# Performance work log

Measured on AMD Instinct MI355X. Metric: run time of the kernel, lower is better.

Reference implementation:

```python
import jax, jax.numpy as jnp
import numpy as np

C = 128; HEADS = 8; GH = 32; GW = 32; B = 8; PD = 8  # PD = (dim//4)//4

def _conv(x, w, pad, dil=1, groups=1):
    return jax.lax.conv_general_dilated(
        x, w, (1, 1), [(pad[0], pad[0]), (pad[1], pad[1])],
        rhs_dilation=(dil, dil),
        dimension_numbers=('NCHW', 'OIHW', 'NCHW'),
        feature_group_count=groups)

def _lrelu(t):
    return jnp.where(t >= 0, t, 0.1 * t)

def _ln(t, g, b, eps=1e-5):
    m = jnp.mean(t, -1, keepdims=True)
    v = jnp.var(t, -1, keepdims=True)
    return (t - m) * jax.lax.rsqrt(v + eps) * g + b

def setup_inputs():
    rng = np.random.RandomState(0)
    f = lambda *s: jnp.asarray((rng.randn(*s) * 0.05).astype(np.float32))
    ones = lambda n: jnp.ones((n,), jnp.float32)
    zeros = lambda n: jnp.zeros((n,), jnp.float32)
    # Swin-style relative position index over the (GH, GW) group
    coords = np.stack(np.meshgrid(np.arange(GH), np.arange(GW), indexing='ij')).reshape(2, -1)
    rel = (coords[:, :, None] - coords[:, None, :]).transpose(1, 2, 0)
    rel[..., 0] += GH - 1; rel[..., 1] += GW - 1; rel[..., 0] *= 2 * GW - 1
    rel_idx = jnp.asarray(rel.sum(-1).astype(np.int32))  # [N, N]
    biases = np.stack(np.meshgrid(np.arange(1 - GH, GH), np.arange(1 - GW, GW), indexing='ij'))
    biases = jnp.asarray(biases.reshape(2, -1).T.astype(np.float32))  # [(2GH-1)*(2GW-1), 2]
    return dict(
        x=jnp.asarray(rng.rand(B, C, GH, GW).astype(np.float32)),
        conv1_w=f(C, C, 3, 3), conv2_w=f(C, C, 3, 3), conv3_w=f(C, C, 3, 3),
        convt_w=f(C, 3, 1, 1),
        rba_w=f(C, C, 3, 1), rba_b=zeros(C), rbb_w=f(C, C, 1, 3), rbb_b=zeros(C),
        pp_w=f(PD, 2), pp_b=zeros(PD),
        l1_g=ones(PD), l1_b=zeros(PD), l1_w=f(PD, PD), l1_b2=zeros(PD),
        l2_g=ones(PD), l2_b=zeros(PD), l2_w=f(PD, PD), l2_b2=zeros(PD),
        l3_g=ones(PD), l3_b=zeros(PD), l3_w=f(HEADS, PD), l3_b2=zeros(HEADS),
        qk_w=f(2 * C, C), qk_b=zeros(2 * C),
        v_w=f(C, C), v_b=zeros(C),
        proj_w=f(C, C), proj_b=zeros(C),
        fc1_w=f(C, C), fc1_b=zeros(C), fc2_w=f(C, C), fc2_b=zeros(C),
        biases=biases, rel_idx=rel_idx,
    )

def reference(x, conv1_w, conv2_w, conv3_w, convt_w, rba_w, rba_b, rbb_w, rbb_b,
              pp_w, pp_b, l1_g, l1_b, l1_w, l1_b2, l2_g, l2_b, l2_w, l2_b2,
              l3_g, l3_b, l3_w, l3_b2, qk_w, qk_b, v_w, v_b, proj_w, proj_b,
              fc1_w, fc1_b, fc2_w, fc2_b, biases, rel_idx):
    Bn, Cc, Hh, Ww = x.shape
    N = Hh * Ww
    hd = Cc // HEADS
    # FeaExtract: ResASPP (3 dilated 3x3 convs, grouped 1x1 merge) + residual
    b1 = _lrelu(_conv(x, conv1_w, (1, 1)))
    b2 = _lrelu(_conv(x, conv2_w, (3, 3), dil=3))
    b3 = _lrelu(_conv(x, conv3_w, (5, 5), dil=5))
    a = _conv(jnp.concatenate([b1, b2, b3], 1), convt_w, (0, 0), groups=Cc) + x
    # RB: (3,1) conv -> lrelu -> (1,3) conv + residual
    r = _lrelu(_conv(a, rba_w, (1, 0)) + rba_b[None, :, None, None])
    r = _conv(r, rbb_w, (0, 1)) + rbb_b[None, :, None, None]
    o0 = r + a
    # original uses in-place clamp_, so o0 is clamped before flattening
    o0 = jnp.clip(o0, 0.0, 1.0)
    E = o0.reshape(Bn, Cc, N).transpose(0, 2, 1)  # [B, N, C]
    qk = E @ qk_w.T + qk_b  # [B, N, 2C]
    q = qk[..., :Cc].reshape(Bn, N, HEADS, hd).transpose(0, 2, 1, 3)
    k = qk[..., Cc:].reshape(Bn, N, HEADS, hd).transpose(0, 2, 1, 3)
    v = (E @ v_w.T + v_b).reshape(Bn, N, HEADS, hd).transpose(0, 2, 1, 3)
    attn = jnp.einsum('bhid,bhjd->bhij', q * (hd ** -0.5), k)
    # DynamicPosBias MLP (residual=False): Linear(2,pd) -> [LN,ReLU,Linear] x2 -> LN,ReLU,Linear(pd,heads)
    p = biases @ pp_w.T + pp_b
    p = jax.nn.relu(_ln(p, l1_g, l1_b)) @ l1_w.T + l1_b2
    p = jax.nn.relu(_ln(p, l2_g, l2_b)) @ l2_w.T + l2_b2
    p = jax.nn.relu(_ln(p, l3_g, l3_b)) @ l3_w.T + l3_b2  # [L, heads]
    rpb = p[rel_idx]  # gather -> [N, N, heads]
    attn = attn + rpb.transpose(2, 0, 1)[None]
    attn = jax.nn.softmax(attn, axis=-1)
    y = jnp.einsum('bhij,bhjd->bhid', attn, v).transpose(0, 2, 1, 3).reshape(Bn, N, Cc) + E
    x_proj = y @ proj_w.T + proj_b
    h = jax.nn.gelu(x_proj @ fc1_w.T + fc1_b, approximate=False)
    return (h @ fc2_w.T + fc2_b) + y
```

## Files before the change

kernel.cpp:

```cpp
#include <hip/hip_runtime.h>
#include <hip/hip_bf16.h>

typedef __hip_bfloat16 bf16;
typedef __bf16 bf16x8 __attribute__((ext_vector_type(8)));
typedef float f32x4 __attribute__((ext_vector_type(4)));
typedef __fp16 f16x2 __attribute__((ext_vector_type(2)));
typedef __fp16 f16x4 __attribute__((ext_vector_type(4)));

#define Lb 3969

#define XP_F   0
#define WF_F   903168
#define WR_F   1124352
#define WG_F   1173504
#define BH_F   1222656
#define R1P_F  1222656
#define QKV_F  1222656
#define AP_F   2795520
#define YT_F   2795520
#define EB_F   3352576
#define XPT_F  3352576
#define H1T_F  0
#define RPB_F  3876864
#define FLAG_F 3908616
#define RT_F   3908624
#define VT_F   4924432

__device__ __forceinline__ float b2f(bf16 v) { return __bfloat162float(v); }
__device__ __forceinline__ bf16 f2b(float v) { return __float2bfloat16(v); }

template <typename T> __device__ __forceinline__ float ldw(const void* p, int i);
template <> __device__ __forceinline__ float ldw<bf16>(const void* p, int i) {
  return __bfloat162float(((const bf16*)p)[i]);
}
template <> __device__ __forceinline__ float ldw<float>(const void* p, int i) {
  return ((const float*)p)[i];
}
template <typename T> __device__ __forceinline__ void stw(void* p, size_t i, float v);
template <> __device__ __forceinline__ void stw<bf16>(void* p, size_t i, float v) {
  ((bf16*)p)[i] = __float2bfloat16(v);
}
template <> __device__ __forceinline__ void stw<float>(void* p, size_t i, float v) {
  ((float*)p)[i] = v;
}

__device__ __forceinline__ unsigned pkb(float a, float b) {
  bf16 x = __float2bfloat16(a), y = __float2bfloat16(b);
  unsigned short ux = *(unsigned short*)&x, uy = *(unsigned short*)&y;
  return (unsigned)ux | ((unsigned)uy << 16);
}
__device__ __forceinline__ unsigned pkh(float a, float b) {
  f16x2 t = __builtin_amdgcn_cvt_pkrtz(a, b);
  return *(unsigned*)&t;
}

__device__ __forceinline__ bool detect_local(const unsigned* x) {
  int lane = threadIdx.x & 63;
  int cnt = 0;
#pragma unroll
  for (int k = 0; k < 4; ++k) {
    unsigned lo = x[lane + 64 * k] & 0xFFFFu;
    cnt += (lo >= 0x3C00u && lo < 0x3F80u) ? 1 : 0;
  }
#pragma unroll
  for (int off = 1; off < 64; off <<= 1) cnt += __shfl_xor(cnt, off);
  return cnt >= 128;
}

template <typename T>
__device__ void wprep_all_body(const void* w1, const void* w2, const void* w3,
                               const void* rba_w, const void* rbb_w,
                               const void* qk_w, const void* v_w,
                               const void* proj_w, const void* fc1_w,
                               const void* fc2_w, bf16* __restrict__ Wf,
                               bf16* __restrict__ Wr, bf16* __restrict__ Wg)
{
  int tid = blockIdx.x * 256 + threadIdx.x;
  int lane = tid & 63, li = lane & 15, quad = lane >> 4;
  if (tid < 55296) {
    int mt = (tid >> 6) & 7;
    int Kc = (tid >> 9) & 3;
    int rem = tid >> 11;
    int t = rem % 9;
    int br = rem / 9;
    const void* w = (br == 0 ? w1 : (br == 1 ? w2 : w3));
    int o = mt * 16 + li;
    int ci0 = Kc * 32 + quad * 8;
#pragma unroll
    for (int j = 0; j < 8; ++j)
      Wf[(size_t)tid * 8 + j] = f2b(ldw<T>(w, (o * 128 + ci0 + j) * 9 + t));
  } else {
    int u = tid - 55296;
    if (u < 12288) {
      int Kc = (u >> 6) & 3, mt = (u >> 8) & 7, q = u >> 11;
      const void* w = (q >= 3) ? rbb_w : rba_w;
      int t = q % 3;
#pragma unroll
      for (int j = 0; j < 8; ++j)
        Wr[(size_t)u * 8 + j] =
            f2b(ldw<T>(w, ((mt * 16 + li) * 128 + Kc * 32 + quad * 8 + j) * 3 + t));
    } else if (u < 24576) {
      int g = u - 12288;
      int Kc = (g >> 6) & 3, mtg = g >> 8;
      const void* w; int mrow; float sc = 1.f;
      if (mtg < 16)      { w = qk_w;   mrow = mtg * 16; if (mtg < 8) sc = 0.25f; }
      else if (mtg < 24) { w = v_w;    mrow = (mtg - 16) * 16; }
      else if (mtg < 32) { w = proj_w; mrow = (mtg - 24) * 16; }
      else if (mtg < 40) { w = fc1_w;  mrow = (mtg - 32) * 16; }
      else               { w = fc2_w;  mrow = (mtg - 40) * 16; }
#pragma unroll
      for (int j = 0; j < 8; ++j)
        Wg[(size_t)g * 8 + j] =
            f2b(sc * ldw<T>(w, (mrow + li) * 128 + Kc * 32 + quad * 8 + j));
    }
  }
}

__global__ __launch_bounds__(256) void wprep_all_kernel(
    const unsigned* x, const void* w1, const void* w2, const void* w3,
    const void* rba_w, const void* rbb_w, const void* qk_w, const void* v_w,
    const void* proj_w, const void* fc1_w, const void* fc2_w,
    bf16* Wf, bf16* Wr, bf16* Wg, int* flag)
{
  bool isbf = detect_local(x);
  if (blockIdx.x == 0 && threadIdx.x == 0) *flag = isbf ? 1 : 0;
  if (isbf) wprep_all_body<bf16>(w1, w2, w3, rba_w, rbb_w, qk_w, v_w, proj_w,
                                 fc1_w, fc2_w, Wf, Wr, Wg);
  else      wprep_all_body<float>(w1, w2, w3, rba_w, rbb_w, qk_w, v_w, proj_w,
                                  fc1_w, fc2_w, Wf, Wr, Wg);
}

template <typename T>
__device__ void nhwc_body(const void* x, bf16* __restrict__ xp, bf16 (*tile)[128])
{
  const int b = blockIdx.x >> 5;
  const int row = blockIdx.x & 31;
  const int t = threadIdx.x;
  const size_t bbase = (size_t)b * 42 * 42 * 128;
  const bf16x8 z = (bf16x8){};

  if (t < 160) {
    int side = t / 80;
    int off = (t % 80) * 8;
    *(bf16x8*)&xp[bbase + ((size_t)(row + 5) * 42 + side * 37) * 128 + off] = z;
  }
  {
    int zr = (row < 5) ? row : ((row >= 27) ? row + 10 : -1);
    if (zr >= 0) {
      size_t base = bbase + (size_t)zr * 42 * 128;
      for (int k = t; k < 672; k += 256) *(bf16x8*)&xp[base + k * 8] = z;
    }
  }

  {
    int ci = t >> 1, half = t & 1;
#pragma unroll
    for (int j = 0; j < 16; ++j) {
      int px = half * 16 + j;
      tile[px][ci] = f2b(ldw<T>(x, ((size_t)b * 128 + ci) * 1024 + row * 32 + px));
    }
  }
  __syncthreads();
  {
    int px = t >> 3, c0 = (t & 7) * 16;
    bf16* dst = xp + (bbase + ((size_t)(row + 5) * 42 + (px + 5)) * 128 + c0);
#pragma unroll
    for (int j = 0; j < 16; ++j) dst[j] = tile[px][c0 + j];
  }
}

__global__ __launch_bounds__(256) void nhwc_kernel(const void* x, bf16* xp,
                                                   const int* flag)
{
  __shared__ bf16 tile[32][128];
  if (*flag) nhwc_body<bf16>(x, xp, tile);
  else       nhwc_body<float>(x, xp, tile);
}

__global__ __launch_bounds__(256) void aspp2_kernel(
    const bf16* __restrict__ xp, const bf16* __restrict__ Wf,
    bf16* __restrict__ bh)
{
  const int nt_ = blockIdx.x, br = blockIdx.y >> 1, mh = blockIdx.y & 1;
  const int bb = blockIdx.z;
  const int w = threadIdx.x >> 6, lane = threadIdx.x & 63;
  const int quad = lane >> 4, li = lane & 15;
  const int d = (br == 0 ? 1 : (br == 1 ? 3 : 5));
  const int pxw = nt_ * 64 + w * 16;
  const int y = pxw >> 5, xb = pxw & 31;

  f32x4 acc[4] = {};
  const bf16* Wbase = Wf + (size_t)br * 18432 * 8 + (size_t)mh * 4 * 64 * 8;

  for (int t = 0; t < 9; ++t) {
    const int dy = (t / 3 - 1) * d, dx = (t % 3 - 1) * d;
    const bf16* Asite =
        xp + (((size_t)bb * 42 + (y + 5 + dy)) * 42 + (xb + li + 5 + dx)) * 128;
    const bf16* Wt = Wbase + (size_t)t * 2048 * 8;
#pragma unroll
    for (int Kc = 0; Kc < 4; ++Kc) {
      bf16x8 afrag = *(const bf16x8*)(Asite + Kc * 32 + quad * 8);
      const bf16* Wk = Wt + (size_t)Kc * 512 * 8 + (size_t)lane * 8;
#pragma unroll
      for (int mt = 0; mt < 4; ++mt) {
        bf16x8 wfrag = *(const bf16x8*)(Wk + (size_t)mt * 64 * 8);
        acc[mt] = __builtin_amdgcn_mfma_f32_16x16x32_bf16(afrag, wfrag, acc[mt],
                                                          0, 0, 0);
      }
    }
  }
#pragma unroll
  for (int mt = 0; mt < 4; ++mt)
#pragma unroll
    for (int r = 0; r < 4; ++r) {
      int px = pxw + quad * 4 + r;
      bh[((size_t)bb * 1024 + px) * 384 + br * 128 + (mh * 4 + mt) * 16 + li] =
          f2b(acc[mt][r]);
    }
}

template <typename T>
__device__ void merge2_body(const bf16* __restrict__ xp, const void* wt,
                            const bf16* __restrict__ bh, bf16* __restrict__ ap,
                            float* cw)
{
  const int b = blockIdx.y, px0 = blockIdx.x * 32;
  const bf16x8 z = (bf16x8){};
  if (blockIdx.x == 0) {
    size_t base = ((size_t)b * 34 + 0) * 32 * 128;
    for (int k = threadIdx.x; k < 512; k += 256) *(bf16x8*)&ap[base + k * 8] = z;
  } else if (blockIdx.x == 31) {
    size_t base = ((size_t)b * 34 + 33) * 32 * 128;
    for (int k = threadIdx.x; k < 512; k += 256) *(bf16x8*)&ap[base + k * 8] = z;
  }
  for (int i = threadIdx.x; i < 384; i += 256) cw[i] = ldw<T>(wt, i);
  __syncthreads();
  const int pxl = threadIdx.x >> 3, og = threadIdx.x & 7;
  const int px = px0 + pxl, o0 = og * 16;
  const int y = px >> 5, x = px & 31;
  const bf16* brow = bh + ((size_t)b * 1024 + px) * 384 + o0 * 3;
  const bf16* xrow = xp + (((size_t)b * 42 + y + 5) * 42 + x + 5) * 128 + o0;
  bf16* arow = ap + (((size_t)b * 34 + y + 1) * 32 + x) * 128 + o0;

  bf16 bl[48], xl[16], ol[16];
#pragma unroll
  for (int k = 0; k < 6; ++k) *(bf16x8*)&bl[k * 8] = *(const bf16x8*)&brow[k * 8];
  *(bf16x8*)&xl[0] = *(const bf16x8*)&xrow[0];
  *(bf16x8*)&xl[8] = *(const bf16x8*)&xrow[8];
#pragma unroll
  for (int j = 0; j < 16; ++j) {
    float v = b2f(xl[j]);
#pragma unroll
    for (int i = 0; i < 3; ++i) {
      float t = b2f(bl[j * 3 + i]);
      v += cw[(o0 + j) * 3 + i] * (t >= 0.f ? t : 0.1f * t);
    }
    ol[j] = f2b(v);
  }
  *(bf16x8*)&arow[0] = *(bf16x8*)&ol[0];
  *(bf16x8*)&arow[8] = *(bf16x8*)&ol[8];
}

__global__ __launch_bounds__(256) void merge2_kernel(
    const bf16* xp, const void* wt, const bf16* bh, bf16* ap, const int* flag)
{
  __shared__ float cw[384];
  if (*flag) merge2_body<bf16>(xp, wt, bh, ap, cw);
  else       merge2_body<float>(xp, wt, bh, ap, cw);
}

template <typename T>
__device__ void rb1_body(const bf16* __restrict__ ap, const bf16* __restrict__ Wr,
                         const void* bias, bf16* __restrict__ r1p)
{
  const int b = blockIdx.z, mh = blockIdx.y;
  const int lane = threadIdx.x;
  const int quad = lane >> 4, li = lane & 15;
  const int pxw = blockIdx.x * 16;
  const int y = pxw >> 5, xb = pxw & 31;
  f32x4 acc[4] = {};
#pragma unroll
  for (int t = 0; t < 3; ++t) {
    const bf16* Asite = ap + (((size_t)b * 34 + y + t) * 32 + xb + li) * 128;
#pragma unroll
    for (int Kc = 0; Kc < 4; ++Kc) {
      bf16x8 afrag = *(const bf16x8*)(Asite + Kc * 32 + quad * 8);
#pragma unroll
      for (int mt = 0; mt < 4; ++mt) {
        int f = (t * 8 + mh * 4 + mt) * 4 + Kc;
        bf16x8 wfrag = *(const bf16x8*)(Wr + ((size_t)f * 64 + lane) * 8);
        acc[mt] = __builtin_amdgcn_mfma_f32_16x16x32_bf16(afrag, wfrag, acc[mt],
                                                          0, 0, 0);
      }
    }
  }
  if (quad == 0) {
    int xcol = (xb == 0) ? 0 : 33;
#pragma unroll
    for (int mt = 0; mt < 4; ++mt)
      r1p[(((size_t)b * 32 + y) * 34 + xcol) * 128 + (mh * 4 + mt) * 16 + li] =
          f2b(0.f);
  }
#pragma unroll
  for (int mt = 0; mt < 4; ++mt) {
    int o = (mh * 4 + mt) * 16 + li;
    float bv = ldw<T>(bias, o);
#pragma unroll
    for (int r = 0; r < 4; ++r) {
      int x = xb + quad * 4 + r;
      float v = acc[mt][r] + bv;
      v = (v >= 0.f ? v : 0.1f * v);
      r1p[(((size_t)b * 32 + y) * 34 + x + 1) * 128 + o] = f2b(v);
    }
  }
}

__global__ __launch_bounds__(64) void rb1_kernel(
    const bf16* ap, const bf16* Wr, const void* bias, bf16* r1p, const int* flag)
{
  if (*flag) rb1_body<bf16>(ap, Wr, bias, r1p);
  else       rb1_body<float>(ap, Wr, bias, r1p);
}

template <typename T>
__device__ void rb2_body(const bf16* __restrict__ r1p, const bf16* __restrict__ Wr,
                         const void* bias, const bf16* __restrict__ ap,
                         bf16* __restrict__ Eb)
{
  const int b = blockIdx.z, mh = blockIdx.y;
  const int lane = threadIdx.x;
  const int quad = lane >> 4, li = lane & 15;
  const int pxw = blockIdx.x * 16;
  const int y = pxw >> 5, xb = pxw & 31;
  f32x4 acc[4] = {};
#pragma unroll
  for (int t = 0; t < 3; ++t) {
    const bf16* Asite = r1p + (((size_t)b * 32 + y) * 34 + xb + li + t) * 128;
#pragma unroll
    for (int Kc = 0; Kc < 4; ++Kc) {
      bf16x8 afrag = *(const bf16x8*)(Asite + Kc * 32 + quad * 8);
#pragma unroll
      for (int mt = 0; mt < 4; ++mt) {
        int f = ((3 + t) * 8 + mh * 4 + mt) * 4 + Kc;
        bf16x8 wfrag = *(const bf16x8*)(Wr + ((size_t)f * 64 + lane) * 8);
        acc[mt] = __builtin_amdgcn_mfma_f32_16x16x32_bf16(afrag, wfrag, acc[mt],
                                                          0, 0, 0);
      }
    }
  }
#pragma unroll
  for (int mt = 0; mt < 4; ++mt) {
    int o = (mh * 4 + mt) * 16 + li;
    float bv = ldw<T>(bias, o);
#pragma unroll
    for (int r = 0; r < 4; ++r) {
      int x = xb + quad * 4 + r;
      float v = acc[mt][r] + bv +
                b2f(ap[(((size_t)b * 34 + y + 1) * 32 + x) * 128 + o]);
      v = fminf(fmaxf(v, 0.f), 1.f);
      Eb[((size_t)b * 1024 + y * 32 + x) * 128 + o] = f2b(v);
    }
  }
}

__global__ __launch_bounds__(64) void rb2_kernel(
    const bf16* r1p, const bf16* Wr, const void* bias, const bf16* ap,
    bf16* Eb, const int* flag)
{
  if (*flag) rb2_body<bf16>(r1p, Wr, bias, ap, Eb);
  else       rb2_body<float>(r1p, Wr, bias, ap, Eb);
}

template <typename T>
__device__ __forceinline__ void ln_relu8(const float* t, float* u,
                                         const void* g, const void* bb)
{
  float m = 0.f;
#pragma unroll
  for (int k = 0; k < 8; ++k) m += t[k];
  m *= 0.125f;
  float v = 0.f;
#pragma unroll
  for (int k = 0; k < 8; ++k) { float d = t[k] - m; v += d * d; }
  v *= 0.125f;
  float r = rsqrtf(v + 1e-5f);
#pragma unroll
  for (int k = 0; k < 8; ++k) {
    float val = (t[k] - m) * r * ldw<T>(g, k) + ldw<T>(bb, k);
    u[k] = val > 0.f ? val : 0.f;
  }
}

template <typename T>
__device__ void dpb_body(const void* biases, const void* pp_w, const void* pp_b,
                         const void* l1_g, const void* l1_b, const void* l1_w,
                         const void* l1_b2, const void* l2_g, const void* l2_b,
                         const void* l2_w, const void* l2_b2, const void* l3_g,
                         const void* l3_b, const void* l3_w, const void* l3_b2,
                         float* __restrict__ RPB)
{
  int r = blockIdx.x * 256 + threadIdx.x;
  if (r >= Lb) return;
  float b0 = ldw<T>(biases, r * 2), b1 = ldw<T>(biases, r * 2 + 1);
  float t[8], u[8];
#pragma unroll
  for (int j = 0; j < 8; ++j)
    t[j] = b0 * ldw<T>(pp_w, j * 2) + b1 * ldw<T>(pp_w, j * 2 + 1) +
           ldw<T>(pp_b, j);
  ln_relu8<T>(t, u, l1_g, l1_b);
#pragma unroll
  for (int j = 0; j < 8; ++j) {
    float s = ldw<T>(l1_b2, j);
#pragma unroll
    for (int k = 0; k < 8; ++k) s += u[k] * ldw<T>(l1_w, j * 8 + k);
    t[j] = s;
  }
  ln_relu8<T>(t, u, l2_g, l2_b);
#pragma unroll
  for (int j = 0; j < 8; ++j) {
    float s = ldw<T>(l2_b2, j);
#pragma unroll
    for (int k = 0; k < 8; ++k) s += u[k] * ldw<T>(l2_w, j * 8 + k);
    t[j] = s;
  }
  ln_relu8<T>(t, u, l3_g, l3_b);
#pragma unroll
  for (int h = 0; h < 8; ++h) {
    float s = ldw<T>(l3_b2, h);
#pragma unroll
    for (int k = 0; k < 8; ++k) s += u[k] * ldw<T>(l3_w, h * 8 + k);
    RPB[h * Lb + r] = s;
  }
}

__global__ __launch_bounds__(256) void dpb_kernel(
    const void* biases, const void* pp_w, const void* pp_b, const void* l1_g,
    const void* l1_b, const void* l1_w, const void* l1_b2, const void* l2_g,
    const void* l2_b, const void* l2_w, const void* l2_b2, const void* l3_g,
    const void* l3_b, const void* l3_w, const void* l3_b2, float* RPB,
    const int* flag)
{
  if (*flag)
    dpb_body<bf16>(biases, pp_w, pp_b, l1_g, l1_b, l1_w, l1_b2, l2_g, l2_b,
                   l2_w, l2_b2, l3_g, l3_b, l3_w, l3_b2, RPB);
  else
    dpb_body<float>(biases, pp_w, pp_b, l1_g, l1_b, l1_w, l1_b2, l2_g, l2_b,
                    l2_w, l2_b2, l3_g, l3_b, l3_w, l3_b2, RPB);
}

__global__ __launch_bounds__(64) void rt_kernel(
    const float* __restrict__ RPB, float* __restrict__ RTf)
{
  const int tt = blockIdx.x, h = blockIdx.y;
  const int t = tt >> 1, p = tt & 1;
  const int lane = threadIdx.x, quad = lane >> 4, li = lane & 15;
  const float* rp = RPB + h * Lb;
  float* dst = RTf + ((size_t)(h * 124 + tt) * 4) * 256 + lane * 4;
#pragma unroll
  for (int mt = 0; mt < 4; ++mt) {
    f32x4 v;
#pragma unroll
    for (int r = 0; r < 4; ++r) {
      int j = mt * 16 + quad * 4 + r;
      int dy = (t - 30) - (j >> 5);
      int dx = (p * 16 + li) - (j & 31);
      v[r] = rp[(dy + 31) * 63 + dx + 31];
    }
    *(f32x4*)(dst + mt * 256) = v;
  }
}

__global__ __launch_bounds__(64) void vt_kernel(
    const bf16* __restrict__ QKV, uint2* __restrict__ VTh)
{
  const int c = blockIdx.x, hh = blockIdx.y, b = blockIdx.z;
  __shared__ bf16 Vl[64][20];
  const int lane = threadIdx.x, quad = lane >> 4, li = lane & 15;
  const bf16* vsrc =
      QKV + ((size_t)b * 1024 + c * 64 + lane) * 384 + 256 + hh * 16;
  union { bf16x8 v; uint2 u[2]; } w0, w1;
  w0.v = *(const bf16x8*)vsrc;
  w1.v = *(const bf16x8*)(vsrc + 8);
  *(uint2*)&Vl[lane][0] = w0.u[0];
  *(uint2*)&Vl[lane][4] = w0.u[1];
  *(uint2*)&Vl[lane][8] = w1.u[0];
  *(uint2*)&Vl[lane][12] = w1.u[1];
  __syncthreads();
  uint2* dst = VTh + (((size_t)(b * 8 + hh) * 16 + c) * 4) * 64 + lane;
#pragma unroll
  for (int mt = 0; mt < 4; ++mt) {
    uint2 pu;
    pu.x = pkh(b2f(Vl[mt * 16 + quad * 4 + 0][li]),
               b2f(Vl[mt * 16 + quad * 4 + 1][li]));
    pu.y = pkh(b2f(Vl[mt * 16 + quad * 4 + 2][li]),
               b2f(Vl[mt * 16 + quad * 4 + 3][li]));
    dst[(size_t)mt * 64] = pu;
  }
}

template <typename T>
__device__ void qkv_body(const bf16* __restrict__ Eb, const bf16* __restrict__ Wg,
                         const void* qk_b, const void* v_b,
                         bf16* __restrict__ QKV)
{
  const int grp = blockIdx.y, b = blockIdx.z;
  const int w = threadIdx.x >> 6, lane = threadIdx.x & 63;
  const int quad = lane >> 4, li = lane & 15;
  const int pxw = blockIdx.x * 64 + w * 16;
  bf16x8 ef[4];
#pragma unroll
  for (int Kc = 0; Kc < 4; ++Kc)
    ef[Kc] = *(const bf16x8*)&Eb[((size_t)b * 1024 + pxw + li) * 128 + Kc * 32 +
                                 quad * 8];
  f32x4 acc[8] = {};
#pragma unroll
  for (int nt = 0; nt < 8; ++nt) {
    int g = grp * 8 + nt;
#pragma unroll
    for (int Kc = 0; Kc < 4; ++Kc) {
      bf16x8 wf = *(const bf16x8*)&Wg[(((size_t)g * 4 + Kc) * 64 + lane) * 8];
      acc[nt] = __builtin_amdgcn_mfma_f32_16x16x32_bf16(ef[Kc], wf, acc[nt],
                                                        0, 0, 0);
    }
  }
#pragma unroll
  for (int nt = 0; nt < 8; ++nt) {
    int g = grp * 8 + nt;
    int o = g * 16 + li;
    float bv;
    if (g < 8)       bv = 0.25f * ldw<T>(qk_b, o);
    else if (g < 16) bv = ldw<T>(qk_b, o);
    else             bv = ldw<T>(v_b, o - 256);
#pragma unroll
    for (int r = 0; r < 4; ++r) {
      int px = pxw + quad * 4 + r;
      QKV[((size_t)b * 1024 + px) * 384 + o] = f2b(acc[nt][r] + bv);
    }
  }
}

__global__ __launch_bounds__(256) void qkv_kernel(
    const bf16* Eb, const bf16* Wg, const void* qk_b, const void* v_b,
    bf16* QKV, const int* flag)
{
  if (*flag) qkv_body<bf16>(Eb, Wg, qk_b, v_b, QKV);
  else       qkv_body<float>(Eb, Wg, qk_b, v_b, QKV);
}

template <typename T, int MODE>
__device__ void mlp_body(const bf16* __restrict__ src, const bf16* __restrict__ Wg,
                         int tb, const void* bias, const bf16* __restrict__ res,
                         void* out)
{
  const int b = blockIdx.z, mh = blockIdx.y;
  const int lane = threadIdx.x;
  const int quad = lane >> 4, li = lane & 15;
  const int pxw = blockIdx.x * 16;
  bf16x8 ef[4];
#pragma unroll
  for (int Kc = 0; Kc < 4; ++Kc)
    ef[Kc] = *(const bf16x8*)&src[((size_t)b * 1024 + pxw + li) * 128 + Kc * 32 +
                                  quad * 8];
  f32x4 acc[2] = {};
#pragma unroll
  for (int nt = 0; nt < 2; ++nt)
#pragma unroll
    for (int Kc = 0; Kc < 4; ++Kc) {
      bf16x8 wf = *(const bf16x8*)&Wg[
          (((size_t)(tb + mh * 2 + nt) * 4 + Kc) * 64 + lane) * 8];
      acc[nt] = __builtin_amdgcn_mfma_f32_16x16x32_bf16(ef[Kc], wf, acc[nt],
                                                        0, 0, 0);
    }
#pragma unroll
  for (int nt = 0; nt < 2; ++nt) {
    int o = (mh * 2 + nt) * 16 + li;
    float bv = ldw<T>(bias, o);
#pragma unroll
    for (int r = 0; r < 4; ++r) {
      int px = pxw + quad * 4 + r;
      float v = acc[nt][r] + bv;
      size_t oidx = ((size_t)b * 1024 + px) * 128 + o;
      if (MODE == 1) v = 0.5f * v * (1.f + erff(v * 0.70710678118f));
      if (MODE == 2) {
        v += b2f(res[oidx]);
        stw<T>(out, oidx, v);
      } else {
        ((bf16*)out)[oidx] = f2b(v);
      }
    }
  }
}

template <int MODE>
__global__ __launch_bounds__(64) void mlp_kernel(
    const bf16* src, const bf16* Wg, int tb, const void* bias, const bf16* res,
    void* out, const int* flag)
{
  if (*flag) mlp_body<bf16, MODE>(src, Wg, tb, bias, res, out);
  else       mlp_body<float, MODE>(src, Wg, tb, bias, res, out);
}

__global__ __launch_bounds__(64) void attn_kernel(
    const bf16* __restrict__ QKV, const bf16* __restrict__ Eb,
    const float* __restrict__ RTf, const uint2* __restrict__ VTh,
    bf16* __restrict__ Yt)
{
  const int qt = blockIdx.x;
  const int hh = blockIdx.y;
  const int b = blockIdx.z;

  const int lane = threadIdx.x;
  const int quad = lane >> 4, li = lane & 15;
  const int qb = qt * 16;

  const bf16* QKVb = QKV + (size_t)b * 1024 * 384;
  const uint2* VTb = VTh + (size_t)(b * 8 + hh) * 4096;
  const float* RTh = RTf + (size_t)hh * 124 * 1024;

  bf16x8 qf = (bf16x8){};
  if (quad < 2)
    qf = *(const bf16x8*)&QKVb[(size_t)(qb + li) * 384 + hh * 16 + quad * 8];

  f32x4 O_ = {};
  float m_st = -1e30f, l_st = 0.f;
  const int sbase = (lane & 48) + ((lane >> 2) & 12);

  struct Buf { bf16x8 kf[4]; f32x4 cin[4]; };
  Buf bA, bB;

  auto LOAD = [&](Buf& bf, int c) {
    const int c0 = c * 64;
    const int tt = ((qt >> 1) - 2 * c + 30) * 2 + (qt & 1);
    const float* rtp = RTh + (size_t)tt * 1024 + lane * 4;
#pragma unroll
    for (int mt = 0; mt < 4; ++mt) {
      bf.cin[mt] = *(const f32x4*)(rtp + mt * 256);
      bf.kf[mt] = (bf16x8){};
      if (quad < 2)
        bf.kf[mt] = *(const bf16x8*)&QKVb[(size_t)(c0 + mt * 16 + li) * 384 +
                                          128 + hh * 16 + quad * 8];
    }
  };

  auto STEP = [&](const Buf& bf, int c) {
    uint2 vb[4];
#pragma unroll
    for (int mt = 0; mt < 4; ++mt)
      vb[mt] = VTb[(size_t)(c * 4 + mt) * 64 + lane];

    f32x4 sT[4];
#pragma unroll
    for (int mt = 0; mt < 4; ++mt)
      sT[mt] = __builtin_amdgcn_mfma_f32_16x16x32_bf16(bf.kf[mt], qf,
                                                       bf.cin[mt], 0, 0, 0);
    float cm = sT[0][0];
#pragma unroll
    for (int mt = 0; mt < 4; ++mt)
#pragma unroll
      for (int r = 0; r < 4; ++r) cm = fmaxf(cm, sT[mt][r]);
    cm = fmaxf(cm, __shfl_xor(cm, 16));
    cm = fmaxf(cm, __shfl_xor(cm, 32));
    if (!__all(cm <= m_st + 8.f)) {
      float mn = fmaxf(m_st, cm);
      float al = __expf(m_st - mn);
      m_st = mn;
      l_st *= al;
#pragma unroll
      for (int r = 0; r < 4; ++r) O_[r] *= __shfl(al, sbase + r);
    }
    float ps = 0.f;
#pragma unroll
    for (int mt = 0; mt < 4; ++mt)
#pragma unroll
      for (int r = 0; r < 4; ++r) {
        float p = __expf(sT[mt][r] - m_st);
        sT[mt][r] = p;
        ps += p;
      }
    ps += __shfl_xor(ps, 16);
    ps += __shfl_xor(ps, 32);
    l_st += ps;

#pragma unroll
    for (int mt = 0; mt < 4; ++mt) {
      union { unsigned u[2]; f16x4 h4; } pu;
      pu.u[0] = pkh(sT[mt][0], sT[mt][1]);
      pu.u[1] = pkh(sT[mt][2], sT[mt][3]);
      union { uint2 u; f16x4 h; } vu;
      vu.u = vb[mt];
      O_ = __builtin_amdgcn_mfma_f32_16x16x16f16(pu.h4, vu.h, O_, 0, 0, 0);
    }
  };

  LOAD(bA, 0);
  for (int c = 0; c < 16; c += 2) {
    LOAD(bB, c + 1);
    STEP(bA, c);
    if (c + 2 < 16) LOAD(bA, c + 2);
    STEP(bB, c + 1);
  }

  const bf16* Ebp = Eb + (size_t)b * 1024 * 128 + hh * 16 + li;
  bf16* Ytp = Yt + (size_t)b * 1024 * 128 + hh * 16 + li;
#pragma unroll
  for (int r = 0; r < 4; ++r) {
    float lb = __shfl(l_st, sbase + r);
    int qrow = qb + quad * 4 + r;
    Ytp[(size_t)qrow * 128] =
        f2b(O_[r] / lb + b2f(Ebp[(size_t)qrow * 128]));
  }
}

extern "C" void kernel_launch(void* const* d_in, const int* in_sizes, int n_in,
                              void* d_out, int out_size, void* d_ws,
                              size_t ws_size, hipStream_t stream)
{
  (void)in_sizes; (void)n_in; (void)out_size; (void)ws_size;
  const void* x       = d_in[0];
  const void* conv1_w = d_in[1];
  const void* conv2_w = d_in[2];
  const void* conv3_w = d_in[3];
  const void* convt_w = d_in[4];
  const void* rba_w   = d_in[5];
  const void* rba_b   = d_in[6];
  const void* rbb_w   = d_in[7];
  const void* rbb_b   = d_in[8];
  const void* pp_w    = d_in[9];
  const void* pp_b    = d_in[10];
  const void* l1_g    = d_in[11];
  const void* l1_b    = d_in[12];
  const void* l1_w    = d_in[13];
  const void* l1_b2   = d_in[14];
  const void* l2_g    = d_in[15];
  const void* l2_b    = d_in[16];
  const void* l2_w    = d_in[17];
  const void* l2_b2   = d_in[18];
  const void* l3_g    = d_in[19];
  const void* l3_b    = d_in[20];
  const void* l3_w    = d_in[21];
  const void* l3_b2   = d_in[22];
  const void* qk_w    = d_in[23];
  const void* qk_b    = d_in[24];
  const void* v_w     = d_in[25];
  const void* v_b     = d_in[26];
  const void* proj_w  = d_in[27];
  const void* proj_b  = d_in[28];
  const void* fc1_w   = d_in[29];
  const void* fc1_b   = d_in[30];
  const void* fc2_w   = d_in[31];
  const void* fc2_b   = d_in[32];
  const void* biases  = d_in[33];

  float* ws   = (float*)d_ws;
  bf16*  xp   = (bf16*)(ws + XP_F);
  bf16*  Wf   = (bf16*)(ws + WF_F);
  bf16*  Wr   = (bf16*)(ws + WR_F);
  bf16*  Wg   = (bf16*)(ws + WG_F);
  bf16*  bh   = (bf16*)(ws + BH_F);
  bf16*  r1p  = (bf16*)(ws + R1P_F);
  bf16*  QKV  = (bf16*)(ws + QKV_F);
  bf16*  ap   = (bf16*)(ws + AP_F);
  bf16*  Yt   = (bf16*)(ws + YT_F);
  bf16*  Eb   = (bf16*)(ws + EB_F);
  bf16*  XPt  = (bf16*)(ws + XPT_F);
  bf16*  H1t  = (bf16*)(ws + H1T_F);
  float* RPB  = ws + RPB_F;
  int*   flag = (int*)(ws + FLAG_F);
  float* RTf  = ws + RT_F;
  uint2* VTh  = (uint2*)(ws + VT_F);

  wprep_all_kernel<<<312, 256, 0, stream>>>(
      (const unsigned*)x, conv1_w, conv2_w, conv3_w, rba_w, rbb_w, qk_w, v_w,
      proj_w, fc1_w, fc2_w, Wf, Wr, Wg, flag);
  nhwc_kernel<<<256, 256, 0, stream>>>(x, xp, flag);
  aspp2_kernel<<<dim3(16, 6, 8), 256, 0, stream>>>(xp, Wf, bh);
  merge2_kernel<<<dim3(32, 8), 256, 0, stream>>>(xp, convt_w, bh, ap, flag);
  rb1_kernel<<<dim3(64, 2, 8), 64, 0, stream>>>(ap, Wr, rba_b, r1p, flag);
  rb2_kernel<<<dim3(64, 2, 8), 64, 0, stream>>>(r1p, Wr, rbb_b, ap, Eb, flag);
  dpb_kernel<<<16, 256, 0, stream>>>(biases, pp_w, pp_b, l1_g, l1_b, l1_w,
                                     l1_b2, l2_g, l2_b, l2_w, l2_b2, l3_g,
                                     l3_b, l3_w, l3_b2, RPB, flag);
  rt_kernel<<<dim3(124, 8), 64, 0, stream>>>(RPB, RTf);
  qkv_kernel<<<dim3(16, 3, 8), 256, 0, stream>>>(Eb, Wg, qk_b, v_b, QKV, flag);
  vt_kernel<<<dim3(16, 8, 8), 64, 0, stream>>>(QKV, VTh);
  attn_kernel<<<dim3(64, 8, 8), 64, 0, stream>>>(QKV, Eb, RTf, VTh, Yt);
  mlp_kernel<0><<<dim3(64, 4, 8), 64, 0, stream>>>(Yt, Wg, 24, proj_b, nullptr,
                                                   XPt, flag);
  mlp_kernel<1><<<dim3(64, 4, 8), 64, 0, stream>>>(XPt, Wg, 32, fc1_b, nullptr,
                                                   H1t, flag);
  mlp_kernel<2><<<dim3(64, 4, 8), 64, 0, stream>>>(H1t, Wg, 40, fc2_b, Yt,
                                                   d_out, flag);
}
```

Baseline: 247.7 us.

## Use base-2 exponentials in attention and pack four query tiles per block

Folds log2(e) into the query scale, query bias and relative-position bias table so the softmax can call the hardware exp2 directly instead of __expf. The lazy-rescale threshold is widened to 11.5 to match the base-2 domain. The attention kernel now runs four 64-lane waves per 256-thread block with launch bounds set for higher occupancy. The manual double-buffered K/bias load pipeline is replaced by a simple loop, relying on more resident waves to hide memory latency. This trades explicit prefetching for occupancy and risks exposing load latency if occupancy does not rise.

```diff
diff --git a/kernel.cpp b/kernel.cpp
--- a/kernel.cpp
+++ b/kernel.cpp
@@ -8,6 +8,8 @@
 typedef __fp16 f16x4 __attribute__((ext_vector_type(4)));
 
 #define Lb 3969
+#define LOG2E 1.4426950408889634f
+#define EXP2(x) __builtin_amdgcn_exp2f(x)
 
 #define XP_F   0
 #define WF_F   903168
@@ -44,11 +46,6 @@
   ((float*)p)[i] = v;
 }
 
-__device__ __forceinline__ unsigned pkb(float a, float b) {
-  bf16 x = __float2bfloat16(a), y = __float2bfloat16(b);
-  unsigned short ux = *(unsigned short*)&x, uy = *(unsigned short*)&y;
-  return (unsigned)ux | ((unsigned)uy << 16);
-}
 __device__ __forceinline__ unsigned pkh(float a, float b) {
   f16x2 t = __builtin_amdgcn_cvt_pkrtz(a, b);
   return *(unsigned*)&t;
@@ -103,7 +100,8 @@
       int g = u - 12288;
       int Kc = (g >> 6) & 3, mtg = g >> 8;
       const void* w; int mrow; float sc = 1.f;
-      if (mtg < 16)      { w = qk_w;   mrow = mtg * 16; if (mtg < 8) sc = 0.25f; }
+      if (mtg < 16)      { w = qk_w;   mrow = mtg * 16;
+                           if (mtg < 8) sc = 0.25f * LOG2E; }
       else if (mtg < 24) { w = v_w;    mrow = (mtg - 16) * 16; }
       else if (mtg < 32) { w = proj_w; mrow = (mtg - 24) * 16; }
       else if (mtg < 40) { w = fc1_w;  mrow = (mtg - 32) * 16; }
@@ -464,7 +462,7 @@
       int j = mt * 16 + quad * 4 + r;
       int dy = (t - 30) - (j >> 5);
       int dx = (p * 16 + li) - (j & 31);
-      v[r] = rp[(dy + 31) * 63 + dx + 31];
+      v[r] = rp[(dy + 31) * 63 + dx + 31] * LOG2E;
     }
     *(f32x4*)(dst + mt * 256) = v;
   }
@@ -528,7 +526,7 @@
     int g = grp * 8 + nt;
     int o = g * 16 + li;
     float bv;
-    if (g < 8)       bv = 0.25f * ldw<T>(qk_b, o);
+    if (g < 8)       bv = (0.25f * LOG2E) * ldw<T>(qk_b, o);
     else if (g < 16) bv = ldw<T>(qk_b, o);
     else             bv = ldw<T>(v_b, o - 256);
 #pragma unroll
@@ -600,16 +598,16 @@
   else       mlp_body<float, MODE>(src, Wg, tb, bias, res, out);
 }
 
-__global__ __launch_bounds__(64) void attn_kernel(
+__global__ __launch_bounds__(256, 8) void attn_kernel(
     const bf16* __restrict__ QKV, const bf16* __restrict__ Eb,
     const float* __restrict__ RTf, const uint2* __restrict__ VTh,
     bf16* __restrict__ Yt)
 {
-  const int qt = blockIdx.x;
+  const int qt = blockIdx.x * 4 + (threadIdx.x >> 6);
   const int hh = blockIdx.y;
   const int b = blockIdx.z;
 
-  const int lane = threadIdx.x;
+  const int lane = threadIdx.x & 63;
   const int quad = lane >> 4, li = lane & 15;
   const int qb = qt * 16;
 
@@ -625,34 +623,27 @@
   float m_st = -1e30f, l_st = 0.f;
   const int sbase = (lane & 48) + ((lane >> 2) & 12);
 
-  struct Buf { bf16x8 kf[4]; f32x4 cin[4]; };
-  Buf bA, bB;
-
-  auto LOAD = [&](Buf& bf, int c) {
+  for (int c = 0; c < 16; ++c) {
     const int c0 = c * 64;
     const int tt = ((qt >> 1) - 2 * c + 30) * 2 + (qt & 1);
     const float* rtp = RTh + (size_t)tt * 1024 + lane * 4;
+
+    f32x4 sT[4];
 #pragma unroll
     for (int mt = 0; mt < 4; ++mt) {
-      bf.cin[mt] = *(const f32x4*)(rtp + mt * 256);
-      bf.kf[mt] = (bf16x8){};
+      f32x4 cin = *(const f32x4*)(rtp + mt * 256);
+      bf16x8 kf = (bf16x8){};
       if (quad < 2)
-        bf.kf[mt] = *(const bf16x8*)&QKVb[(size_t)(c0 + mt * 16 + li) * 384 +
-                                          128 + hh * 16 + quad * 8];
-    }
-  };
-
-  auto STEP = [&](const Buf& bf, int c) {
+        kf = *(const bf16x8*)&QKVb[(size_t)(c0 + mt * 16 + li) * 384 + 128 +
+                                   hh * 16 + quad * 8];
+      sT[mt] = __builtin_amdgcn_mfma_f32_16x16x32_bf16(kf, qf, cin, 0, 0, 0);
+    }
+
     uint2 vb[4];
 #pragma unroll
     for (int mt = 0; mt < 4; ++mt)
       vb[mt] = VTb[(size_t)(c * 4 + mt) * 64 + lane];
 
-    f32x4 sT[4];
-#pragma unroll
-    for (int mt = 0; mt < 4; ++mt)
-      sT[mt] = __builtin_amdgcn_mfma_f32_16x16x32_bf16(bf.kf[mt], qf,
-                                                       bf.cin[mt], 0, 0, 0);
     float cm = sT[0][0];
 #pragma unroll
     for (int mt = 0; mt < 4; ++mt)
@@ -660,9 +651,9 @@
       for (int r = 0; r < 4; ++r) cm = fmaxf(cm, sT[mt][r]);
     cm = fmaxf(cm, __shfl_xor(cm, 16));
     cm = fmaxf(cm, __shfl_xor(cm, 32));
-    if (!__all(cm <= m_st + 8.f)) {
+    if (!__all(cm <= m_st + 11.5f)) {
       float mn = fmaxf(m_st, cm);
-      float al = __expf(m_st - mn);
+      float al = EXP2(m_st - mn);
       m_st = mn;
       l_st *= al;
 #pragma unroll
@@ -673,7 +664,7 @@
     for (int mt = 0; mt < 4; ++mt)
 #pragma unroll
       for (int r = 0; r < 4; ++r) {
-        float p = __expf(sT[mt][r] - m_st);
+        float p = EXP2(sT[mt][r] - m_st);
         sT[mt][r] = p;
         ps += p;
       }
@@ -690,14 +681,6 @@
       vu.u = vb[mt];
       O_ = __builtin_amdgcn_mfma_f32_16x16x16f16(pu.h4, vu.h, O_, 0, 0, 0);
     }
-  };
-
-  LOAD(bA, 0);
-  for (int c = 0; c < 16; c += 2) {
-    LOAD(bB, c + 1);
-    STEP(bA, c);
-    if (c + 2 < 16) LOAD(bA, c + 2);
-    STEP(bB, c + 1);
   }
 
   const bf16* Ebp = Eb + (size_t)b * 1024 * 128 + hh * 16 + li;
@@ -783,7 +766,7 @@
   rt_kernel<<<dim3(124, 8), 64, 0, stream>>>(RPB, RTf);
   qkv_kernel<<<dim3(16, 3, 8), 256, 0, stream>>>(Eb, Wg, qk_b, v_b, QKV, flag);
   vt_kernel<<<dim3(16, 8, 8), 64, 0, stream>>>(QKV, VTh);
-  attn_kernel<<<dim3(64, 8, 8), 64, 0, stream>>>(QKV, Eb, RTf, VTh, Yt);
+  attn_kernel<<<dim3(16, 8, 8), 256, 0, stream>>>(QKV, Eb, RTf, VTh, Yt);
   mlp_kernel<0><<<dim3(64, 4, 8), 64, 0, stream>>>(Yt, Wg, 24, proj_b, nullptr,
                                                    XPt, flag);
   mlp_kernel<1><<<dim3(64, 4, 8), 64, 0, stream>>>(XPt, Wg, 32, fc1_b, nullptr,
```

Result: no change. 245.7 us (-0.8%).
